# Kernel optimization log

Measured on AMD Instinct MI355X. Metric: run time of the kernel, lower is better.

The kernel has to match this reference:

```python
import jax, jax.numpy as jnp
import numpy as np

HIDDEN = 1024
JOINTS = 21
IN_DIM = JOINTS * 3  # 63
BATCH = 64
SEQ = 512


def setup_inputs() -> dict:
    key = jax.random.key(0)
    ks = jax.random.split(key, 11)
    s = 0.02
    f32 = jnp.float32
    return {
        "real_seq": jax.random.normal(ks[0], (BATCH, SEQ, IN_DIM), f32),
        # PyTorch nn.GRU params (gates ordered r, z, n)
        "W_ih": jax.random.normal(ks[1], (3 * HIDDEN, IN_DIM), f32) * s,
        "W_hh": jax.random.normal(ks[2], (3 * HIDDEN, HIDDEN), f32) * s,
        "b_ih": jax.random.normal(ks[3], (3 * HIDDEN,), f32) * s,
        "b_hh": jax.random.normal(ks[4], (3 * HIDDEN,), f32) * s,
        # projector MLP (no nonlinearities in the original)
        "W1": jax.random.normal(ks[5], (HIDDEN, HIDDEN), f32) * s,
        "b1": jax.random.normal(ks[6], (HIDDEN,), f32) * s,
        "W2": jax.random.normal(ks[7], (HIDDEN, HIDDEN), f32) * s,
        "b2": jax.random.normal(ks[8], (HIDDEN,), f32) * s,
        "W3": jax.random.normal(ks[9], (IN_DIM, HIDDEN), f32) * s,
        "b3": jax.random.normal(ks[10], (IN_DIM,), f32) * s,
        "condition_length": 5,
        "ground_truth_length": 5,
    }


def _condition_list(seq_len, condition_length, ground_truth_length):
    gt = np.ones((100, ground_truth_length))
    co = np.zeros((100, condition_length))
    return np.concatenate((gt, co), 1).reshape(-1)[:seq_len]


def reference(real_seq, W_ih, W_hh, b_ih, b_hh, W1, b1, W2, b2, W3, b3,
              condition_length, ground_truth_length):
    B, T, D = real_seq.shape
    H = W_hh.shape[1]
    cond = jnp.asarray(_condition_list(T, condition_length, ground_truth_length),
                       dtype=real_seq.dtype)  # [T], static 1/0 teacher-forcing pattern

    h0 = jnp.zeros((B, H), real_seq.dtype)
    o0 = jnp.zeros((B, D), real_seq.dtype)
    xs = (jnp.transpose(real_seq, (1, 0, 2)), cond)  # time-major

    def step(carry, x):
        h, out = carry
        xt, c = x
        inp = jnp.where(c > 0.5, xt, out)  # teacher-forcing switch
        gi = inp @ W_ih.T + b_ih           # [B, 3H]
        gh = h @ W_hh.T + b_hh             # [B, 3H]
        i_r, i_z, i_n = jnp.split(gi, 3, axis=-1)
        h_r, h_z, h_n = jnp.split(gh, 3, axis=-1)
        r = jax.nn.sigmoid(i_r + h_r)
        z = jax.nn.sigmoid(i_z + h_z)
        n = jnp.tanh(i_n + r * h_n)
        h_new = (1.0 - z) * n + z * h
        lin = (h_new @ W1.T + b1) @ W2.T + b2
        out_new = inp + lin @ W3.T + b3    # residual velocities
        return (h_new, out_new), out_new

    _, outs = jax.lax.scan(step, (h0, o0), xs)  # outs: [T, B, D]
    return jnp.transpose(outs, (1, 0, 2)).reshape(B, T, D // 3, 3)
```

## Files before the change

kernel.cpp:

```cpp
#include <hip/hip_runtime.h>
#include <hip/hip_bf16.h>


#define HIDDEN 1024
#define INDIM  63
#define TSEQ   512
#define MB     16
#define NGRP   4
#define HB_DW  (MB * 1024)

typedef __attribute__((ext_vector_type(8))) short bfrag8;
typedef __attribute__((ext_vector_type(4))) float ffrag4;
typedef __attribute__((ext_vector_type(4))) unsigned u32x4;
typedef unsigned long long ull;

#define MFMA_B16(a, b, c) __builtin_amdgcn_mfma_f32_16x16x32_bf16((a), (b), (c), 0, 0, 0)

#define GLOAD4(dst, ptr) \
  asm volatile("global_load_dwordx4 %0, %1, off sc0 sc1" \
               : "=v"(dst) : "v"(ptr) : "memory")

__device__ __forceinline__ short f2bf(float x) {
  __hip_bfloat16 b = __float2bfloat16(x);
  return __builtin_bit_cast(short, b);
}
__device__ __forceinline__ float bf2f(short s) {
  unsigned u = ((unsigned)(unsigned short)s) << 16;
  return __builtin_bit_cast(float, u);
}


__global__ void k_t1(const float* __restrict__ W2, const float* __restrict__ b1,
                     const float* __restrict__ b2, float* __restrict__ t1) {
  const int w = threadIdx.x >> 6, lane = threadIdx.x & 63;
  const int o = blockIdx.x * 4 + w;
  if (o >= HIDDEN) return;
  const float* row = W2 + (size_t)o * HIDDEN;
  float s = 0.f;
  for (int k = lane; k < HIDDEN; k += 64) s += row[k] * b1[k];
  for (int off = 32; off; off >>= 1) s += __shfl_down(s, off, 64);
  if (lane == 0) t1[o] = s + b2[o];
}

__global__ void k_bp(const float* __restrict__ W3, const float* __restrict__ t1,
                     const float* __restrict__ b3, float* __restrict__ bp) {
  const int w = threadIdx.x >> 6, lane = threadIdx.x & 63;
  for (int d = w; d < INDIM; d += 4) {
    const float* row = W3 + (size_t)d * HIDDEN;
    float s = 0.f;
    for (int k = lane; k < HIDDEN; k += 64) s += row[k] * t1[k];
    for (int off = 32; off; off >>= 1) s += __shfl_down(s, off, 64);
    if (lane == 0) bp[d] = s + b3[d];
  }
}

__global__ void k_gemm(const float* __restrict__ A, const float* __restrict__ B,
                       float* __restrict__ C, int M, int N, int K) {
  __shared__ float As[16][17], Bs[16][17];
  const int tx = threadIdx.x, ty = threadIdx.y;
  const int row = blockIdx.y * 16 + ty;
  const int col = blockIdx.x * 16 + tx;
  float acc = 0.f;
  for (int k0 = 0; k0 < K; k0 += 16) {
    As[ty][tx] = (row < M) ? A[(size_t)row * K + k0 + tx] : 0.f;
    Bs[ty][tx] = B[(size_t)(k0 + ty) * N + col];
    __syncthreads();
#pragma unroll
    for (int kk = 0; kk < 16; ++kk) acc += As[ty][kk] * Bs[kk][tx];
    __syncthreads();
  }
  if (row < M && col < N) C[(size_t)row * N + col] = acc;
}


__global__ __launch_bounds__(256, 1) void k_main(
    const float* __restrict__ X,
    const float* __restrict__ W_ih, const float* __restrict__ W_hh,
    const float* __restrict__ b_ih, const float* __restrict__ b_hh,
    const float* __restrict__ WpF, const float* __restrict__ bpF,
    const int* __restrict__ pCL, const int* __restrict__ pGT,
    unsigned* __restrict__ hb, float* __restrict__ OUT) {
  __shared__ short h_st[MB][HIDDEN + 8];
  __shared__ short inp_bf[MB][88];
  __shared__ float inp_f[MB][68];
  __shared__ float gt_z[MB][20], gt_hn[MB][20];
  __shared__ float gt_ir[MB][20], gt_iz[MB][20], gt_in[MB][20];
  __shared__ short htmp[MB][20];
  __shared__ int pub_flag;

  const int tid = threadIdx.x;
  const int w = tid >> 6;
  const int lane = tid & 63;
  const int c = lane & 15;
  const int quad = lane >> 4;
  const int g = blockIdx.x >> 6;
  const int j = blockIdx.x & 63;

  const int gtv = pGT[0];
  int period = pCL[0] + gtv;
  if (period < 1) period = 1;

  bfrag8 wB[32];
  bfrag8 wp[32];
  if (w < 3) {
    const float* wr = W_hh + ((size_t)w * HIDDEN + (size_t)j * 16 + c) * HIDDEN;
#pragma unroll
    for (int ks = 0; ks < 32; ++ks) {
      const float* p = wr + ks * 32 + quad * 8;
      bfrag8 f;
#pragma unroll
      for (int e = 0; e < 8; ++e) f[e] = f2bf(p[e]);
      wB[ks] = f;
    }
  } else {
#pragma unroll
    for (int gate = 0; gate < 3; ++gate) {
      const float* wr = W_ih + ((size_t)gate * HIDDEN + (size_t)j * 16 + c) * INDIM;
#pragma unroll
      for (int ks = 0; ks < 2; ++ks) {
        bfrag8 f;
#pragma unroll
        for (int e = 0; e < 8; ++e) {
          int k = ks * 32 + quad * 8 + e;
          f[e] = (k < INDIM) ? f2bf(wr[k]) : (short)0;
        }
        wB[gate * 2 + ks] = f;
      }
    }
  }
  const int dd = 16 * w + c;
  {
    const float* wr = WpF + (size_t)dd * HIDDEN;
#pragma unroll
    for (int ks = 0; ks < 32; ++ks) {
      bfrag8 f;
#pragma unroll
      for (int e = 0; e < 8; ++e)
        f[e] = (dd < INDIM) ? f2bf(wr[ks * 32 + quad * 8 + e]) : (short)0;
      wp[ks] = f;
    }
  }

  float bias_g;
  if (w == 0)      bias_g = b_ih[j * 16 + c] + b_hh[j * 16 + c];
  else if (w == 1) bias_g = b_ih[HIDDEN + j * 16 + c] + b_hh[HIDDEN + j * 16 + c];
  else if (w == 2) bias_g = b_hh[2 * HIDDEN + j * 16 + c];
  else             bias_g = b_ih[2 * HIDDEN + j * 16 + c];
  const float bp_l = (dd < INDIM) ? bpF[dd] : 0.f;

  for (int i = tid; i < MB * (HIDDEN + 8); i += 256) ((short*)h_st)[i] = 0;
  for (int i = tid; i < MB * 88; i += 256) ((short*)inp_bf)[i] = 0;
  for (int i = tid; i < MB * 68; i += 256) ((float*)inp_f)[i] = 0.f;
  if (tid == 0) pub_flag = 0;

  unsigned* hb_g[2] = {hb + (size_t)g * HB_DW,
                       hb + (size_t)(NGRP + g) * HB_DW};

  const int xrow = tid >> 4, xd0 = (tid & 15) * 4;
  float xp[4];
  if ((0 % period) < gtv) {
    const float* xr = X + ((size_t)(g * MB + xrow) * TSEQ + 0) * INDIM;
#pragma unroll
    for (int e = 0; e < 4; ++e) xp[e] = (xd0 + e < INDIM) ? xr[xd0 + e] : 0.f;
  }

  for (int t = 0; t < TSEQ; ++t) {
    const unsigned tg = (unsigned)(t + 1);
    const bool teach = ((t % period) < gtv);
    if (teach) {
#pragma unroll
      for (int e = 0; e < 4; ++e) {
        inp_f[xrow][xd0 + e] = xp[e];
        inp_bf[xrow][xd0 + e] = f2bf(xp[e]);
      }
    }
    __syncthreads();

    ffrag4 ghr;
    float hp[4];
    if (w < 3) {
      ffrag4 acc[4];
#pragma unroll
      for (int e = 0; e < 4; ++e) {
        acc[0][e] = bias_g; acc[1][e] = 0.f; acc[2][e] = 0.f; acc[3][e] = 0.f;
      }
#pragma unroll
      for (int ks = 0; ks < 32; ++ks) {
        const bfrag8 a = *(const bfrag8*)&h_st[c][ks * 32 + quad * 8];
        acc[ks & 3] = MFMA_B16(a, wB[ks], acc[ks & 3]);
      }
      ffrag4 gsum = acc[0] + acc[1] + acc[2] + acc[3];
      if (w == 1) {
#pragma unroll
        for (int i = 0; i < 4; ++i) gt_z[quad * 4 + i][c] = gsum[i];
      } else if (w == 2) {
#pragma unroll
        for (int i = 0; i < 4; ++i) gt_hn[quad * 4 + i][c] = gsum[i];
      } else {
        ghr = gsum;
#pragma unroll
        for (int i = 0; i < 4; ++i) hp[i] = bf2f(h_st[quad * 4 + i][j * 16 + c]);
      }
    } else {
      ffrag4 gir, giz, gin;
#pragma unroll
      for (int e = 0; e < 4; ++e) { gir[e] = 0.f; giz[e] = 0.f; gin[e] = bias_g; }
#pragma unroll
      for (int ks = 0; ks < 2; ++ks) {
        const bfrag8 a = *(const bfrag8*)&inp_bf[c][ks * 32 + quad * 8];
        gir = MFMA_B16(a, wB[0 + ks], gir);
        giz = MFMA_B16(a, wB[2 + ks], giz);
        gin = MFMA_B16(a, wB[4 + ks], gin);
      }
#pragma unroll
      for (int i = 0; i < 4; ++i) {
        gt_ir[quad * 4 + i][c] = gir[i];
        gt_iz[quad * 4 + i][c] = giz[i];
        gt_in[quad * 4 + i][c] = gin[i];
      }
    }
    __syncthreads();

    unsigned* hw = hb_g[t & 1];
    if (w == 0) {
#pragma unroll
      for (int i = 0; i < 4; ++i) {
        const int row = quad * 4 + i;
        float r = 1.f / (1.f + __expf(-(ghr[i] + gt_ir[row][c])));
        float z = 1.f / (1.f + __expf(-(gt_z[row][c] + gt_iz[row][c])));
        float n = tanhf(gt_in[row][c] + r * gt_hn[row][c]);
        htmp[row][c] = f2bf((1.f - z) * n + z * hp[i]);
      }
      asm volatile("" ::: "memory");
      const int r = lane >> 2, q4 = (lane & 3) * 4;
      unsigned d0 = ((unsigned)tg << 16) | (unsigned)(unsigned short)htmp[r][q4 + 0];
      unsigned d1 = ((unsigned)tg << 16) | (unsigned)(unsigned short)htmp[r][q4 + 1];
      unsigned d2 = ((unsigned)tg << 16) | (unsigned)(unsigned short)htmp[r][q4 + 2];
      unsigned d3 = ((unsigned)tg << 16) | (unsigned)(unsigned short)htmp[r][q4 + 3];
      ull w0v = ((ull)d1 << 32) | d0;
      ull w1v = ((ull)d3 << 32) | d2;
      ull* dst = (ull*)(hw + (size_t)r * 1024 + 16 * j + q4);
      __hip_atomic_store(dst, w0v, __ATOMIC_RELAXED, __HIP_MEMORY_SCOPE_SYSTEM);
      __hip_atomic_store(dst + 1, w1v, __ATOMIC_RELAXED, __HIP_MEMORY_SCOPE_SYSTEM);
      asm volatile("" ::: "memory");
      if (lane == 0) *(volatile int*)&pub_flag = (int)tg;
    } else {
      while (*(volatile int*)&pub_flag < (int)tg) __builtin_amdgcn_s_sleep(1);
    }

    {
      const int tn = t + 1;
      if (tn < TSEQ && ((tn % period) < gtv)) {
        const float* xr = X + ((size_t)(g * MB + xrow) * TSEQ + tn) * INDIM;
#pragma unroll
        for (int e = 0; e < 4; ++e) xp[e] = (xd0 + e < INDIM) ? xr[xd0 + e] : 0.f;
      }
    }

    {
      u32x4 v[16];
      const unsigned* gp = hw + (size_t)tid * 4;
#pragma unroll
      for (int s = 0; s < 16; ++s) GLOAD4(v[s], gp + s * 1024);
      asm volatile("s_waitcnt vmcnt(0)" ::: "memory");
      __builtin_amdgcn_sched_barrier(0);

      unsigned bad = 0;
#pragma unroll
      for (int s = 0; s < 16; ++s) {
        if ((v[s][0] >> 16) != tg || (v[s][1] >> 16) != tg ||
            (v[s][2] >> 16) != tg || (v[s][3] >> 16) != tg)
          bad |= (1u << s);
      }
      while (__ballot(bad != 0)) {
#pragma unroll
        for (int s = 0; s < 16; ++s) {
          if (__ballot((bad >> s) & 1u)) GLOAD4(v[s], gp + s * 1024);
        }
        asm volatile("s_waitcnt vmcnt(0)" ::: "memory");
        __builtin_amdgcn_sched_barrier(0);
        bad = 0;
#pragma unroll
        for (int s = 0; s < 16; ++s) {
          if ((v[s][0] >> 16) != tg || (v[s][1] >> 16) != tg ||
              (v[s][2] >> 16) != tg || (v[s][3] >> 16) != tg)
            bad |= (1u << s);
        }
      }
#pragma unroll
      for (int s = 0; s < 16; ++s) {
        const int ci = tid + s * 256;
        const int row = ci >> 8;
        const int cb = (ci & 255) * 4;
        ull p = (ull)(v[s][0] & 0xFFFFu) | ((ull)(v[s][1] & 0xFFFFu) << 16) |
                ((ull)(v[s][2] & 0xFFFFu) << 32) | ((ull)(v[s][3] & 0xFFFFu) << 48);
        *(ull*)&h_st[row][cb] = p;
      }
    }
    __syncthreads();

    const int wj = t & 63;
    const bool rep = (t + 1 < TSEQ) && !(((t + 1) % period) < gtv);
    if (rep || j == wj) {
      ffrag4 oa0, oa1;
#pragma unroll
      for (int e = 0; e < 4; ++e) { oa0[e] = bp_l; oa1[e] = 0.f; }
#pragma unroll
      for (int ks = 0; ks < 32; ++ks) {
        const bfrag8 a = *(const bfrag8*)&h_st[c][ks * 32 + quad * 8];
        if (ks & 1) oa1 = MFMA_B16(a, wp[ks], oa1);
        else        oa0 = MFMA_B16(a, wp[ks], oa0);
      }
      ffrag4 o = oa0 + oa1;
#pragma unroll
      for (int i = 0; i < 4; ++i) {
        const int row = quad * 4 + i;
        if (dd < INDIM) {
          float val = o[i] + inp_f[row][dd];
          if (j == wj) OUT[((size_t)(g * MB + row) * TSEQ + t) * INDIM + dd] = val;
          if (rep) { inp_f[row][dd] = val; inp_bf[row][dd] = f2bf(val); }
        } else if (rep) {
          inp_bf[row][dd] = 0;
        }
      }
    }
  }
}


extern "C" void kernel_launch(void* const* d_in, const int* in_sizes, int n_in,
                              void* d_out, int out_size, void* d_ws, size_t ws_size,
                              hipStream_t stream) {
  const float* X    = (const float*)d_in[0];
  const float* W_ih = (const float*)d_in[1];
  const float* W_hh = (const float*)d_in[2];
  const float* b_ih = (const float*)d_in[3];
  const float* b_hh = (const float*)d_in[4];
  const float* W1   = (const float*)d_in[5];
  const float* b1   = (const float*)d_in[6];
  const float* W2   = (const float*)d_in[7];
  const float* b2   = (const float*)d_in[8];
  const float* W3   = (const float*)d_in[9];
  const float* b3   = (const float*)d_in[10];
  const int* pCL    = (const int*)d_in[11];
  const int* pGT    = (const int*)d_in[12];
  float* OUT = (float*)d_out;

  char* ws = (char*)d_ws;
  float* bp = (float*)(ws + 1024);
  float* t1 = (float*)(ws + 2048);
  float* Wp = (float*)(ws + 8192);
  float* T2 = (float*)(ws + 270336);
  unsigned* hb = (unsigned*)(ws + 270336);
  if (ws_size < 795 * 1024) return;

  k_t1<<<256, 256, 0, stream>>>(W2, b1, b2, t1);
  k_gemm<<<dim3(64, 4), dim3(16, 16), 0, stream>>>(W3, W2, T2, INDIM, HIDDEN, HIDDEN);
  k_gemm<<<dim3(64, 4), dim3(16, 16), 0, stream>>>(T2, W1, Wp, INDIM, HIDDEN, HIDDEN);
  k_bp<<<1, 256, 0, stream>>>(W3, t1, b3, bp);
  hipMemsetAsync(hb, 0, (size_t)2 * NGRP * HB_DW * sizeof(unsigned), stream);
  k_main<<<256, 256, 0, stream>>>(X, W_ih, W_hh, b_ih, b_hh, Wp, bp, pCL, pGT, hb, OUT);
}
```

Before: 3.354 ms.

## Replace per-element tagged hidden-state exchange with packed data plus per-block flags

Hidden-state publication now stores packed bf16 values without per-element step tags, which halves the exchange buffer. Each block raises a per-block flag after its stores complete, and readers poll 64 flags before loading the packed state. Removing the tag check and the repack shrinks global traffic and the work in the spin loop, at the cost of an extra flag round trip and a vmcnt wait on the writer. The intra-block LDS publish flag is removed, so the other waves no longer wait for wave 0 and rely on the global flag poll instead.

```diff
diff --git a/kernel.cpp b/kernel.cpp
--- a/kernel.cpp
+++ b/kernel.cpp
@@ -7,7 +7,7 @@
 #define TSEQ   512
 #define MB     16
 #define NGRP   4
-#define HB_DW  (MB * 1024)
+#define HB_DW  (MB * 512)
 
 typedef __attribute__((ext_vector_type(8))) short bfrag8;
 typedef __attribute__((ext_vector_type(4))) float ffrag4;
@@ -79,14 +79,14 @@
     const float* __restrict__ b_ih, const float* __restrict__ b_hh,
     const float* __restrict__ WpF, const float* __restrict__ bpF,
     const int* __restrict__ pCL, const int* __restrict__ pGT,
-    unsigned* __restrict__ hb, float* __restrict__ OUT) {
+    unsigned* __restrict__ hb, unsigned* __restrict__ fl,
+    float* __restrict__ OUT) {
   __shared__ short h_st[MB][HIDDEN + 8];
   __shared__ short inp_bf[MB][88];
   __shared__ float inp_f[MB][68];
   __shared__ float gt_z[MB][20], gt_hn[MB][20];
   __shared__ float gt_ir[MB][20], gt_iz[MB][20], gt_in[MB][20];
   __shared__ short htmp[MB][20];
-  __shared__ int pub_flag;
 
   const int tid = threadIdx.x;
   const int w = tid >> 6;
@@ -151,10 +151,11 @@
   for (int i = tid; i < MB * (HIDDEN + 8); i += 256) ((short*)h_st)[i] = 0;
   for (int i = tid; i < MB * 88; i += 256) ((short*)inp_bf)[i] = 0;
   for (int i = tid; i < MB * 68; i += 256) ((float*)inp_f)[i] = 0.f;
-  if (tid == 0) pub_flag = 0;
 
   unsigned* hb_g[2] = {hb + (size_t)g * HB_DW,
                        hb + (size_t)(NGRP + g) * HB_DW};
+  unsigned* fg = fl + g * 64;
+  const unsigned* fladdr = fg + (lane & 15) * 4;
 
   const int xrow = tid >> 4, xd0 = (tid & 15) * 4;
   float xp[4];
@@ -232,20 +233,17 @@
         htmp[row][c] = f2bf((1.f - z) * n + z * hp[i]);
       }
       asm volatile("" ::: "memory");
-      const int r = lane >> 2, q4 = (lane & 3) * 4;
-      unsigned d0 = ((unsigned)tg << 16) | (unsigned)(unsigned short)htmp[r][q4 + 0];
-      unsigned d1 = ((unsigned)tg << 16) | (unsigned)(unsigned short)htmp[r][q4 + 1];
-      unsigned d2 = ((unsigned)tg << 16) | (unsigned)(unsigned short)htmp[r][q4 + 2];
-      unsigned d3 = ((unsigned)tg << 16) | (unsigned)(unsigned short)htmp[r][q4 + 3];
-      ull w0v = ((ull)d1 << 32) | d0;
-      ull w1v = ((ull)d3 << 32) | d2;
-      ull* dst = (ull*)(hw + (size_t)r * 1024 + 16 * j + q4);
-      __hip_atomic_store(dst, w0v, __ATOMIC_RELAXED, __HIP_MEMORY_SCOPE_SYSTEM);
-      __hip_atomic_store(dst + 1, w1v, __ATOMIC_RELAXED, __HIP_MEMORY_SCOPE_SYSTEM);
-      asm volatile("" ::: "memory");
-      if (lane == 0) *(volatile int*)&pub_flag = (int)tg;
-    } else {
-      while (*(volatile int*)&pub_flag < (int)tg) __builtin_amdgcn_s_sleep(1);
+      const int r = lane >> 2, li = lane & 3, q4 = li * 4;
+      ull pv = (ull)(unsigned short)htmp[r][q4 + 0] |
+               ((ull)(unsigned short)htmp[r][q4 + 1] << 16) |
+               ((ull)(unsigned short)htmp[r][q4 + 2] << 32) |
+               ((ull)(unsigned short)htmp[r][q4 + 3] << 48);
+      __hip_atomic_store((ull*)hw + (size_t)r * 256 + j * 4 + li, pv,
+                         __ATOMIC_RELAXED, __HIP_MEMORY_SCOPE_SYSTEM);
+      asm volatile("s_waitcnt vmcnt(0)" ::: "memory");
+      if (lane == 0)
+        __hip_atomic_store(&fg[j], tg, __ATOMIC_RELAXED,
+                           __HIP_MEMORY_SCOPE_SYSTEM);
     }
 
     {
@@ -258,43 +256,28 @@
     }
 
     {
-      u32x4 v[16];
-      const unsigned* gp = hw + (size_t)tid * 4;
-#pragma unroll
-      for (int s = 0; s < 16; ++s) GLOAD4(v[s], gp + s * 1024);
+      for (;;) {
+        u32x4 fv;
+        GLOAD4(fv, fladdr);
+        asm volatile("s_waitcnt vmcnt(0)" ::: "memory");
+        __builtin_amdgcn_sched_barrier(0);
+        const bool ok = fv[0] >= tg && fv[1] >= tg && fv[2] >= tg && fv[3] >= tg;
+        if (__ballot(!ok) == 0ull) break;
+        __builtin_amdgcn_s_sleep(1);
+      }
+
+      u32x4 v[8];
+      const unsigned* gp = hw;
+#pragma unroll
+      for (int s = 0; s < 8; ++s) GLOAD4(v[s], gp + (size_t)(s * 256 + tid) * 4);
       asm volatile("s_waitcnt vmcnt(0)" ::: "memory");
       __builtin_amdgcn_sched_barrier(0);
-
-      unsigned bad = 0;
-#pragma unroll
-      for (int s = 0; s < 16; ++s) {
-        if ((v[s][0] >> 16) != tg || (v[s][1] >> 16) != tg ||
-            (v[s][2] >> 16) != tg || (v[s][3] >> 16) != tg)
-          bad |= (1u << s);
-      }
-      while (__ballot(bad != 0)) {
-#pragma unroll
-        for (int s = 0; s < 16; ++s) {
-          if (__ballot((bad >> s) & 1u)) GLOAD4(v[s], gp + s * 1024);
-        }
-        asm volatile("s_waitcnt vmcnt(0)" ::: "memory");
-        __builtin_amdgcn_sched_barrier(0);
-        bad = 0;
-#pragma unroll
-        for (int s = 0; s < 16; ++s) {
-          if ((v[s][0] >> 16) != tg || (v[s][1] >> 16) != tg ||
-              (v[s][2] >> 16) != tg || (v[s][3] >> 16) != tg)
-            bad |= (1u << s);
-        }
-      }
-#pragma unroll
-      for (int s = 0; s < 16; ++s) {
-        const int ci = tid + s * 256;
-        const int row = ci >> 8;
-        const int cb = (ci & 255) * 4;
-        ull p = (ull)(v[s][0] & 0xFFFFu) | ((ull)(v[s][1] & 0xFFFFu) << 16) |
-                ((ull)(v[s][2] & 0xFFFFu) << 32) | ((ull)(v[s][3] & 0xFFFFu) << 48);
-        *(ull*)&h_st[row][cb] = p;
+#pragma unroll
+      for (int s = 0; s < 8; ++s) {
+        const int u = s * 256 + tid;
+        const int row = u >> 7;
+        const int col0 = (u & 127) * 8;
+        *(u32x4*)&h_st[row][col0] = v[s];
       }
     }
     __syncthreads();
@@ -352,12 +335,17 @@
   float* Wp = (float*)(ws + 8192);
   float* T2 = (float*)(ws + 270336);
   unsigned* hb = (unsigned*)(ws + 270336);
+  unsigned* fl = (unsigned*)(ws + 270336 + 2 * NGRP * HB_DW * sizeof(unsigned));
   if (ws_size < 795 * 1024) return;
 
   k_t1<<<256, 256, 0, stream>>>(W2, b1, b2, t1);
   k_gemm<<<dim3(64, 4), dim3(16, 16), 0, stream>>>(W3, W2, T2, INDIM, HIDDEN, HIDDEN);
   k_gemm<<<dim3(64, 4), dim3(16, 16), 0, stream>>>(T2, W1, Wp, INDIM, HIDDEN, HIDDEN);
   k_bp<<<1, 256, 0, stream>>>(W3, t1, b3, bp);
-  hipMemsetAsync(hb, 0, (size_t)2 * NGRP * HB_DW * sizeof(unsigned), stream);
-  k_main<<<256, 256, 0, stream>>>(X, W_ih, W_hh, b_ih, b_hh, Wp, bp, pCL, pGT, hb, OUT);
-}
+  hipMemsetAsync(hb, 0,
+                 (size_t)2 * NGRP * HB_DW * sizeof(unsigned) +
+                     NGRP * 64 * sizeof(unsigned),
+                 stream);
+  k_main<<<256, 256, 0, stream>>>(X, W_ih, W_hh, b_ih, b_hh, Wp, bp, pCL, pGT,
+                                  hb, fl, OUT);
+}
```

New measurement: 3.483 ms. 3.9% more time.
